# Optimization experiments

Hardware: AMD Instinct MI355X
Metric: run time of the kernel (lower is better)

Reference implementation:

```python
import jax, jax.numpy as jnp
import numpy as np

T, B, I, H, O = 512, 128, 256, 1024, 256


def setup_inputs() -> dict:
    key = jax.random.key(0)
    ks = jax.random.split(key, 16)
    std = 0.02
    inp = {
        "input_seq": jax.random.normal(ks[0], (T, B, I), dtype=jnp.float32),
        # encoder LSTM (torch gate order i, f, g, o)
        "W_ih_enc": jax.random.normal(ks[1], (4 * H, I), dtype=jnp.float32) * std,
        "W_hh_enc": jax.random.normal(ks[2], (4 * H, H), dtype=jnp.float32) * std,
        "b_ih_enc": jnp.zeros((4 * H,), dtype=jnp.float32),
        "b_hh_enc": jnp.zeros((4 * H,), dtype=jnp.float32),
        # attention: Linear(2H -> H) and score vector v
        "W_attn": jax.random.normal(ks[3], (H, 2 * H), dtype=jnp.float32) * std,
        "b_attn": jnp.zeros((H,), dtype=jnp.float32),
        "v": jax.random.uniform(ks[4], (H,), dtype=jnp.float32),
        # decoder LSTMCell (H -> H)
        "W_ih_dec": jax.random.normal(ks[5], (4 * H, H), dtype=jnp.float32) * std,
        "W_hh_dec": jax.random.normal(ks[6], (4 * H, H), dtype=jnp.float32) * std,
        "b_ih_dec": jnp.zeros((4 * H,), dtype=jnp.float32),
        "b_hh_dec": jnp.zeros((4 * H,), dtype=jnp.float32),
        # decoder linear H -> H
        "W_dec": jax.random.normal(ks[7], (H, H), dtype=jnp.float32) * std,
        "b_dec": jnp.zeros((H,), dtype=jnp.float32),
        # top-level output linear H -> O
        "W_out": jax.random.normal(ks[8], (O, H), dtype=jnp.float32) * std,
        "b_out": jnp.zeros((O,), dtype=jnp.float32),
        "len_out": 30,
    }
    return inp


def _lstm_cell(h, c, x, Wih, Whh, bih, bhh):
    gates = x @ Wih.T + bih + h @ Whh.T + bhh  # [B, 4H]
    i, f, g, o = jnp.split(gates, 4, axis=-1)
    i, f, o = jax.nn.sigmoid(i), jax.nn.sigmoid(f), jax.nn.sigmoid(o)
    c = f * c + i * jnp.tanh(g)
    h = o * jnp.tanh(c)
    return h, c


def reference(input_seq, W_ih_enc, W_hh_enc, b_ih_enc, b_hh_enc,
              W_attn, b_attn, v, W_ih_dec, W_hh_dec, b_ih_dec, b_hh_dec,
              W_dec, b_dec, W_out, b_out, len_out):
    Tdim, Bdim, _ = input_seq.shape
    Hdim = W_hh_enc.shape[1]

    # ---- encoder LSTM over time (seq-first) ----
    h0 = jnp.zeros((Bdim, Hdim), dtype=input_seq.dtype)
    c0 = jnp.zeros((Bdim, Hdim), dtype=input_seq.dtype)

    def enc_step(carry, x_t):
        h, c = carry
        h, c = _lstm_cell(h, c, x_t, W_ih_enc, W_hh_enc, b_ih_enc, b_hh_enc)
        return (h, c), h

    (h_enc, _), context_seq = jax.lax.scan(enc_step, (h0, c0), input_seq)
    # dropout is identity in eval mode

    # ---- precompute context part of Bahdanau energy ----
    # W_attn acts on cat([hidden, context]) => split into hidden / context blocks
    W_h, W_c = W_attn[:, :Hdim], W_attn[:, Hdim:]
    ctx_proj = jnp.einsum('tbh,gh->tbg', context_seq, W_c) + b_attn  # [T,B,H]

    def dec_step(carry, _):
        h, c = carry
        energy = jnp.tanh(h @ W_h.T + ctx_proj)          # [T,B,H]
        scores = jnp.einsum('tbh,h->tb', energy, v)       # [T,B]
        w = jax.nn.softmax(scores, axis=0)                # softmax over time
        context = jnp.einsum('tbh,tb->bh', context_seq, w)  # [B,H]
        h, c = _lstm_cell(h, c, context, W_ih_dec, W_hh_dec, b_ih_dec, b_hh_dec)
        out = jax.nn.relu(h @ W_dec.T + b_dec)
        out = out @ W_out.T + b_out
        return (h, c), out

    _, outputs = jax.lax.scan(dec_step, (h_enc, jnp.zeros_like(h_enc)), None,
                              length=len_out)
    return outputs  # [len_out, B, O]
```

## Files before the change

kernel.cpp:

```cpp
#include <hip/hip_runtime.h>
#include <hip/hip_bf16.h>
#include <type_traits>


static constexpr int T_ = 512, B_ = 128, I_ = 256, H_ = 1024, O_ = 256;

typedef unsigned short ushort;
typedef unsigned long long u64;
typedef __attribute__((ext_vector_type(8))) short bf16x8;
typedef __attribute__((ext_vector_type(4))) float f32x4;
typedef __attribute__((ext_vector_type(4))) unsigned uint4_t;
typedef __attribute__((ext_vector_type(8))) _Float16 half8;

__device__ __forceinline__ float bf2f(ushort u) {
    union { unsigned i; float f; } cv; cv.i = ((unsigned)u) << 16; return cv.f;
}
__device__ __forceinline__ ushort f2bf(float f) {
    union { float f; unsigned u; } c; c.f = f;
    unsigned r = c.u + 0x7FFFu + ((c.u >> 16) & 1u);
    return (ushort)(r >> 16);
}
__device__ __forceinline__ float fast_sigmoid(float x) { return 1.f / (1.f + __expf(-x)); }
__device__ __forceinline__ float fast_tanh(float x) {
    float ax = fabsf(x);
    float e = __expf(-2.f * ax);
    float t = (1.f - e) / (1.f + e);
    return copysignf(t, x);
}
__device__ __forceinline__ f32x4 mfma16(bf16x8 a, bf16x8 b, f32x4 c) {
    return __builtin_amdgcn_mfma_f32_16x16x32_bf16(a, b, c, 0, 0, 0);
}
__device__ __forceinline__ bf16x8 ld8(const ushort* p) { return *(const bf16x8*)(const void*)p; }

__device__ __forceinline__ bf16x8 ld8p(const ushort* base, int row, int ko) {
    const size_t t = (size_t)(row >> 7);
    const int b = row & 127;
    const ushort* p0 = base + t * (size_t)(B_ * H_) + ((size_t)((ko >> 2) * B_ + b) << 2);
    union { u64 q[2]; bf16x8 v; } u;
    u.q[0] = *(const u64*)(const void*)p0;
    u.q[1] = *(const u64*)(const void*)(p0 + (B_ << 2));
    return u.v;
}

__device__ __forceinline__ void split8(const float* p, bf16x8& hi, bf16x8& lo) {
    #pragma unroll
    for (int j = 0; j < 8; j++) {
        const float f = p[j];
        const ushort h = f2bf(f);
        hi[j] = (short)h;
        lo[j] = (short)f2bf(f - bf2f(h));
    }
}

__global__ __launch_bounds__(256) void split_w(
    const float* __restrict__ src, int srcld, int coloff,
    ushort* __restrict__ hi, ushort* __restrict__ lo, int K)
{
    const int k = blockIdx.x * 256 + threadIdx.x;
    const int r = blockIdx.y;
    const float f = src[(size_t)r * srcld + coloff + k];
    const ushort h = f2bf(f);
    hi[(size_t)r * K + k] = h;
    lo[(size_t)r * K + k] = f2bf(f - bf2f(h));
}

__global__ __launch_bounds__(256) void pack_x(float* __restrict__ x)
{
    const size_t i = ((size_t)blockIdx.x * 256 + threadIdx.x) * 8;
    float4 a = *(const float4*)(x + i);
    float4 b = *(const float4*)(x + i + 4);
    unsigned w[8];
    const float f_[8] = {a.x, a.y, a.z, a.w, b.x, b.y, b.z, b.w};
    #pragma unroll
    for (int j = 0; j < 8; j++) {
        const ushort h = f2bf(f_[j]);
        const ushort l = f2bf(f_[j] - bf2f(h));
        w[j] = (unsigned)h | ((unsigned)l << 16);
    }
    *(uint4_t*)(void*)(x + i)     = uint4_t{w[0], w[1], w[2], w[3]};
    *(uint4_t*)(void*)(x + i + 4) = uint4_t{w[4], w[5], w[6], w[7]};
}

#define ENC_SMEM_BYTES (32*64*8*2*2 + 8*64*8*2*2 + 16*132*4)
#define LORING_SLOTS 256

__global__ __launch_bounds__(512) void enc_persistent(
    const unsigned* __restrict__ xpk,
    const ushort* __restrict__ WhhE_h, const ushort* __restrict__ WhhE_l,
    const ushort* __restrict__ WihE_h, const ushort* __restrict__ WihE_l,
    const float* __restrict__ bih, const float* __restrict__ bhh,
    const ushort* __restrict__ hzero,
    ushort* __restrict__ ctx_seq,
    ushort* __restrict__ loring,
    ushort* __restrict__ enc_lo_fin,
    unsigned* __restrict__ bar)
{
    extern __shared__ __align__(16) char smem[];
    ushort* LWh = (ushort*)smem;
    ushort* LWl = LWh + 32 * 64 * 8;
    ushort* LIh = LWl + 32 * 64 * 8;
    ushort* LIl = LIh + 8 * 64 * 8;
    float*  Gt  = (float*)(LIl + 8 * 64 * 8);

    const int tid  = threadIdx.x;
    const int wave = tid >> 6, lane = tid & 63;
    const int quad = lane >> 4, l15 = lane & 15;
    const int bx   = blockIdx.x;
    const int h0   = bx << 2;
    const int wr   = ((l15 >> 2) * H_) + h0 + (l15 & 3);

    {
        const size_t woff = (size_t)wr * H_;
        #pragma unroll
        for (int ii = 0; ii < 4; ii++) {
            const int i   = wave + (ii << 3);
            const int src = (i << 5) + (quad << 3);
            *(bf16x8*)(LWh + ((i << 6) + lane) * 8) = ld8(WhhE_h + woff + src);
            *(bf16x8*)(LWl + ((i << 6) + lane) * 8) = ld8(WhhE_l + woff + src);
        }
        const size_t ioff = (size_t)wr * I_;
        const int src2 = (wave << 5) + (quad << 3);
        *(bf16x8*)(LIh + ((wave << 6) + lane) * 8) = ld8(WihE_h + ioff + src2);
        *(bf16x8*)(LIl + ((wave << 6) + lane) * 8) = ld8(WihE_l + ioff + src2);
    }

    const int bl_  = tid >> 2, hl = tid & 3;
    const int hidx = h0 + hl;
    const float bs0 = bih[hidx]           + bhh[hidx];
    const float bs1 = bih[H_ + hidx]      + bhh[H_ + hidx];
    const float bs2 = bih[2 * H_ + hidx]  + bhh[2 * H_ + hidx];
    const float bs3 = bih[3 * H_ + hidx]  + bhh[3 * H_ + hidx];
    float c_reg = 0.f;
    __syncthreads();

    const int arow = (wave << 4) + l15;
    const size_t xoff = (size_t)arow * I_;

    for (int t = 0; t < T_; t++) {
        const unsigned* xs = xpk + (size_t)t * (B_ * I_) + xoff;

        f32x4 acc0 = {0.f, 0.f, 0.f, 0.f}, acc1 = acc0, acc2 = acc0;
        #pragma unroll
        for (int kc = 0; kc < I_; kc += 32) {
            const int i = kc >> 5;
            const bf16x8 bh = *(const bf16x8*)(LIh + ((i << 6) + lane) * 8);
            const bf16x8 bl = *(const bf16x8*)(LIl + ((i << 6) + lane) * 8);
            const uint4_t w0 = *(const uint4_t*)(const void*)(xs + kc + (quad << 3));
            const uint4_t w1 = *(const uint4_t*)(const void*)(xs + kc + (quad << 3) + 4);
            bf16x8 ah, al;
            ah[0] = (short)(w0.x & 0xffff); al[0] = (short)(w0.x >> 16);
            ah[1] = (short)(w0.y & 0xffff); al[1] = (short)(w0.y >> 16);
            ah[2] = (short)(w0.z & 0xffff); al[2] = (short)(w0.z >> 16);
            ah[3] = (short)(w0.w & 0xffff); al[3] = (short)(w0.w >> 16);
            ah[4] = (short)(w1.x & 0xffff); al[4] = (short)(w1.x >> 16);
            ah[5] = (short)(w1.y & 0xffff); al[5] = (short)(w1.y >> 16);
            ah[6] = (short)(w1.z & 0xffff); al[6] = (short)(w1.z >> 16);
            ah[7] = (short)(w1.w & 0xffff); al[7] = (short)(w1.w >> 16);
            acc0 = mfma16(ah, bh, acc0);
            acc1 = mfma16(ah, bl, acc1);
            acc2 = mfma16(al, bh, acc2);
        }

        if (t != 0) {
            if (tid == 0) {
                while (__hip_atomic_load(&bar[0], __ATOMIC_RELAXED,
                                         __HIP_MEMORY_SCOPE_AGENT) < (unsigned)t)
                    __builtin_amdgcn_s_sleep(2);
            }
            __syncthreads();
        }

        const ushort* hi_src = t ? (ctx_seq + (size_t)(t - 1) * (B_ * H_)) : hzero;
        const ushort* lo_src = t ? (loring + (size_t)((t - 1) & (LORING_SLOTS - 1))
                                             * (B_ * H_)) : hzero;
        #pragma unroll 8
        for (int kc = 0; kc < H_; kc += 32) {
            const int i  = kc >> 5;
            const int ko = kc + (quad << 3);
            const bf16x8 bh = *(const bf16x8*)(LWh + ((i << 6) + lane) * 8);
            const bf16x8 bl = *(const bf16x8*)(LWl + ((i << 6) + lane) * 8);
            const bf16x8 ah = ld8p(hi_src, arow, ko);
            const bf16x8 al = ld8p(lo_src, arow, ko);
            acc0 = mfma16(ah, bh, acc0);
            acc1 = mfma16(ah, bl, acc1);
            acc2 = mfma16(al, bh, acc2);
        }
        #pragma unroll
        for (int r = 0; r < 4; r++)
            Gt[l15 * 132 + (wave << 4) + (quad << 2) + r] = acc0[r] + acc1[r] + acc2[r];
        __syncthreads();

        const float gi = Gt[hl * 132 + bl_]        + bs0;
        const float gf = Gt[(4 + hl) * 132 + bl_]  + bs1;
        const float gg = Gt[(8 + hl) * 132 + bl_]  + bs2;
        const float go = Gt[(12 + hl) * 132 + bl_] + bs3;
        const float ig = fast_sigmoid(gi), fg = fast_sigmoid(gf);
        const float gtv = fast_tanh(gg),   og = fast_sigmoid(go);
        c_reg = fg * c_reg + ig * gtv;
        const float hnew = og * fast_tanh(c_reg);
        const ushort hh  = f2bf(hnew);
        const ushort hlo = f2bf(hnew - bf2f(hh));

        const unsigned hp = (unsigned)hh  | (__shfl_down((unsigned)hh, 1)  << 16);
        const unsigned lp = (unsigned)hlo | (__shfl_down((unsigned)hlo, 1) << 16);
        const unsigned pi = ((unsigned)bx << 9) + (unsigned)tid;
        if (!(tid & 1)) {
            __hip_atomic_store((unsigned*)(void*)&ctx_seq[(size_t)t * (B_ * H_) + pi],
                               hp, __ATOMIC_RELAXED, __HIP_MEMORY_SCOPE_AGENT);
            __hip_atomic_store((unsigned*)(void*)
                               &loring[(size_t)(t & (LORING_SLOTS - 1)) * (B_ * H_) + pi],
                               lp, __ATOMIC_RELAXED, __HIP_MEMORY_SCOPE_AGENT);
            if (t == T_ - 1)
                *(unsigned*)(void*)&enc_lo_fin[pi] = lp;
        }

        if (t != T_ - 1) {
            __syncthreads();
            if (tid == 0) {
                const unsigned tgt = (unsigned)(t + 1) * 16u;
                unsigned* leaf = bar + 64 + ((bx & 15) << 4);
                const unsigned la = __hip_atomic_fetch_add(leaf, 1u, __ATOMIC_RELAXED,
                                                           __HIP_MEMORY_SCOPE_AGENT) + 1;
                if (la == tgt) {
                    const unsigned ra = __hip_atomic_fetch_add(&bar[32], 1u,
                                            __ATOMIC_RELAXED, __HIP_MEMORY_SCOPE_AGENT) + 1;
                    if (ra == tgt)
                        __hip_atomic_store(&bar[0], (unsigned)(t + 1),
                                           __ATOMIC_RELAXED, __HIP_MEMORY_SCOPE_AGENT);
                }
            }
        }
    }
}

template<bool WSPLIT, bool XSPLIT, int KX>
__global__ __launch_bounds__(256) void lstm_mfma(
    const ushort* __restrict__ h_hi, const ushort* __restrict__ h_lo,
    const void* __restrict__ x_p, const ushort* __restrict__ x_lo,
    const void* __restrict__ Whh_a, const void* __restrict__ Whh_b,
    const void* __restrict__ Wih_a, const void* __restrict__ Wih_b,
    const float* __restrict__ bih, const float* __restrict__ bhh,
    const float* __restrict__ c_in, float* __restrict__ c_out,
    ushort* __restrict__ h_out_hi, ushort* __restrict__ h_out_lo)
{
    __shared__ float Gt[16][65];
    const int tid = threadIdx.x;
    const int wave = tid >> 6, lane = tid & 63;
    const int quad = lane >> 4, l15 = lane & 15;
    const int h0 = blockIdx.x << 2;
    const int mbase = (blockIdx.y << 6) + (wave << 4);
    const int arow = mbase + l15;
    const int wr = ((l15 >> 2) * H_) + h0 + (l15 & 3);

    f32x4 acc0 = {0.f,0.f,0.f,0.f}, acc1 = acc0, acc2 = acc0;

    {
        const size_t woff = (size_t)wr * H_;
        #pragma unroll 4
        for (int kc = 0; kc < H_; kc += 32) {
            const int ko = kc + quad * 8;
            bf16x8 bh, bl;
            if constexpr (WSPLIT) {
                bh = ld8((const ushort*)Whh_a + woff + ko);
                bl = ld8((const ushort*)Whh_b + woff + ko);
            } else {
                split8((const float*)Whh_a + woff + ko, bh, bl);
            }
            const bf16x8 ah = ld8p(h_hi, arow, ko);
            const bf16x8 al = ld8p(h_lo, arow, ko);
            acc0 = mfma16(ah, bh, acc0);
            acc1 = mfma16(ah, bl, acc1);
            acc2 = mfma16(al, bh, acc2);
        }
    }
    {
        const size_t woff = (size_t)wr * KX;
        #pragma unroll 2
        for (int kc = 0; kc < KX; kc += 32) {
            const int ko = kc + quad * 8;
            bf16x8 bh, bl;
            if constexpr (WSPLIT) {
                bh = ld8((const ushort*)Wih_a + woff + ko);
                bl = ld8((const ushort*)Wih_b + woff + ko);
            } else {
                split8((const float*)Wih_a + woff + ko, bh, bl);
            }
            bf16x8 ah, al;
            if constexpr (XSPLIT) {
                ah = ld8p((const ushort*)x_p, arow, ko);
                al = ld8p(x_lo, arow, ko);
            } else {
                split8((const float*)x_p + (size_t)arow * KX + ko, ah, al);
            }
            acc0 = mfma16(ah, bh, acc0);
            acc1 = mfma16(ah, bl, acc1);
            acc2 = mfma16(al, bh, acc2);
        }
    }
    #pragma unroll
    for (int r = 0; r < 4; r++)
        Gt[l15][(wave << 4) + quad * 4 + r] = acc0[r] + acc1[r] + acc2[r];
    __syncthreads();

    const int bl_ = tid >> 2, hl = tid & 3;
    const int b = (blockIdx.y << 6) + bl_;
    const int hidx = h0 + hl;
    const float gi = Gt[hl][bl_]      + bih[hidx]          + bhh[hidx];
    const float gf = Gt[4 + hl][bl_]  + bih[H_ + hidx]     + bhh[H_ + hidx];
    const float gg = Gt[8 + hl][bl_]  + bih[2 * H_ + hidx] + bhh[2 * H_ + hidx];
    const float go = Gt[12 + hl][bl_] + bih[3 * H_ + hidx] + bhh[3 * H_ + hidx];
    const float ig = fast_sigmoid(gi), fg = fast_sigmoid(gf);
    const float gt = fast_tanh(gg),    og = fast_sigmoid(go);
    const float cold = c_in[b * H_ + hidx];
    const float cnew = fg * cold + ig * gt;
    const float hnew = og * fast_tanh(cnew);
    c_out[b * H_ + hidx] = cnew;
    const ushort hh = f2bf(hnew);
    const size_t op = ((size_t)(hidx >> 2) * B_ + b) * 4 + (hidx & 3);
    h_out_hi[op] = hh;
    h_out_lo[op] = f2bf(hnew - bf2f(hh));
}

template<bool A_LO, int NT, int OM, bool RELU, int K, bool APANEL>
__global__ __launch_bounds__(256) void gemm_mfma(
    const ushort* __restrict__ Ahi, const ushort* __restrict__ Alo, int lda,
    const ushort* __restrict__ Whi, const ushort* __restrict__ Wlo,
    const float* __restrict__ bias,
    void* __restrict__ out0, void* __restrict__ out1, int ldc)
{
    const int tid = threadIdx.x;
    const int wave = tid >> 6, lane = tid & 63;
    const int quad = lane >> 4, l15 = lane & 15;
    const int colbase = (blockIdx.x * NT) << 4;
    const int row = (blockIdx.y << 6) + (wave << 4) + l15;
    const size_t aoff = (size_t)row * lda;

    f32x4 acc0[NT], acc1[NT], acc2[NT];
    #pragma unroll
    for (int nt = 0; nt < NT; nt++) {
        acc0[nt] = {0.f,0.f,0.f,0.f}; acc1[nt] = acc0[nt]; acc2[nt] = acc0[nt];
    }
    size_t woff[NT];
    #pragma unroll
    for (int nt = 0; nt < NT; nt++)
        woff[nt] = (size_t)(colbase + (nt << 4) + l15) * K;

    #pragma unroll 2
    for (int kc = 0; kc < K; kc += 32) {
        const int ko = kc + quad * 8;
        const bf16x8 ah = APANEL ? ld8p(Ahi, row, ko) : ld8(Ahi + aoff + ko);
        bf16x8 al;
        if (A_LO) al = APANEL ? ld8p(Alo, row, ko) : ld8(Alo + aoff + ko);
        #pragma unroll
        for (int nt = 0; nt < NT; nt++) {
            const bf16x8 bh = ld8(Whi + woff[nt] + ko);
            const bf16x8 bl = ld8(Wlo + woff[nt] + ko);
            acc0[nt] = mfma16(ah, bh, acc0[nt]);
            acc1[nt] = mfma16(ah, bl, acc1[nt]);
            if (A_LO) acc2[nt] = mfma16(al, bh, acc2[nt]);
        }
    }
    const size_t orow0 = ((size_t)blockIdx.y << 6) + (wave << 4) + quad * 4;
    const size_t HALF_IDX = (size_t)32768 * 1024;
    #pragma unroll
    for (int nt = 0; nt < NT; nt++) {
        const int col = colbase + (nt << 4) + l15;
        const float bv = bias ? bias[col] : 0.f;
        #pragma unroll
        for (int r = 0; r < 4; r++) {
            float v = acc0[nt][r] + acc1[nt][r] + (A_LO ? acc2[nt][r] : 0.f) + bv;
            if (RELU) v = fmaxf(v, 0.f);
            const size_t idx = (orow0 + r) * (size_t)ldc + col;
            if constexpr (OM == 0) {
                ((float*)out0)[idx] = v;
            } else if constexpr (OM == 3) {
                const size_t idxp = ((size_t)(col >> 2) * B_ + (orow0 + r)) * 4 + (col & 3);
                const ushort h = f2bf(v);
                ((ushort*)out0)[idxp] = h;
                ((ushort*)out1)[idxp] = f2bf(v - bf2f(h));
            } else {
                if (idx < HALF_IDX) ((_Float16*)out0)[idx] = (_Float16)v;
                else                ((_Float16*)out1)[idx - HALF_IDX] = (_Float16)v;
            }
        }
    }
}

__global__ __launch_bounds__(256) void attn_score_kernel(
    const float* __restrict__ q,
    const _Float16* __restrict__ P0, const _Float16* __restrict__ P1,
    const float* __restrict__ v, float* __restrict__ scores)
{
    const int wave = threadIdx.x >> 6, lane = threadIdx.x & 63;
    const int p = (blockIdx.x << 2) + wave;
    const int t = p >> 7, b = p & 127;
    const size_t base = (size_t)(t * B_ + b) * H_ + (lane << 4);
    const size_t HALF_IDX = (size_t)32768 * 1024;
    const _Float16* pp = (base < HALF_IDX) ? (P0 + base) : (P1 + (base - HALF_IDX));

    const half8 u0 = *(const half8*)(const void*)pp;
    const half8 u1 = *(const half8*)(const void*)(pp + 8);
    float pv[16];
    #pragma unroll
    for (int j = 0; j < 8; j++) { pv[j] = (float)u0[j]; pv[8 + j] = (float)u1[j]; }

    const float* qp = q + b * H_ + (lane << 4);
    const float* vp = v + (lane << 4);
    float sum = 0.f;
    #pragma unroll
    for (int j0 = 0; j0 < 16; j0 += 4) {
        const float4 qv = *(const float4*)(qp + j0);
        const float4 vv = *(const float4*)(vp + j0);
        sum += vv.x * fast_tanh(qv.x + pv[j0 + 0]);
        sum += vv.y * fast_tanh(qv.y + pv[j0 + 1]);
        sum += vv.z * fast_tanh(qv.z + pv[j0 + 2]);
        sum += vv.w * fast_tanh(qv.w + pv[j0 + 3]);
    }
    #pragma unroll
    for (int off = 32; off; off >>= 1) sum += __shfl_down(sum, off);
    if (lane == 0) scores[b * T_ + t] = sum;
}

__global__ __launch_bounds__(256) void softmax_kernel(
    const float* __restrict__ scores, float* __restrict__ scT)
{
    __shared__ float red[256];
    const int b = blockIdx.x, tid = threadIdx.x;
    const float s0 = scores[b * T_ + tid];
    const float s1 = scores[b * T_ + tid + 256];
    red[tid] = fmaxf(s0, s1);
    __syncthreads();
    for (int off = 128; off; off >>= 1) {
        if (tid < off) red[tid] = fmaxf(red[tid], red[tid + off]);
        __syncthreads();
    }
    const float mx = red[0];
    __syncthreads();
    const float e0 = __expf(s0 - mx), e1 = __expf(s1 - mx);
    red[tid] = e0 + e1;
    __syncthreads();
    for (int off = 128; off; off >>= 1) {
        if (tid < off) red[tid] += red[tid + off];
        __syncthreads();
    }
    const float inv = 1.f / red[0];
    scT[tid * B_ + b] = e0 * inv;
    scT[(tid + 256) * B_ + b] = e1 * inv;
}

__global__ __launch_bounds__(256) void attn_context_kernel(
    const float* __restrict__ scT, const ushort* __restrict__ ctx,
    ushort* __restrict__ chi, ushort* __restrict__ clo)
{
    const int u = blockIdx.x * 256 + threadIdx.x;
    const int c = u >> 7, b = u & 127;
    const ushort* cp = ctx + ((size_t)(c * B_ + b) << 2);
    const float* wp = scT + b;
    float a0 = 0.f, a1 = 0.f, a2 = 0.f, a3 = 0.f;
    #pragma unroll 4
    for (int t = 0; t < T_; t++) {
        const float w = wp[t << 7];
        const u64 raw = *(const u64*)(const void*)(cp + (size_t)t * (B_ * H_));
        a0 += w * bf2f((ushort)raw);
        a1 += w * bf2f((ushort)(raw >> 16));
        a2 += w * bf2f((ushort)(raw >> 32));
        a3 += w * bf2f((ushort)(raw >> 48));
    }
    const size_t i0 = (size_t)(c * B_ + b) << 2;
    const ushort h0 = f2bf(a0), h1 = f2bf(a1), h2 = f2bf(a2), h3 = f2bf(a3);
    const ushort l0 = f2bf(a0 - bf2f(h0)), l1 = f2bf(a1 - bf2f(h1));
    const ushort l2 = f2bf(a2 - bf2f(h2)), l3 = f2bf(a3 - bf2f(h3));
    *(u64*)(void*)&chi[i0] = (u64)h0 | ((u64)h1 << 16) | ((u64)h2 << 32) | ((u64)h3 << 48);
    *(u64*)(void*)&clo[i0] = (u64)l0 | ((u64)l1 << 16) | ((u64)l2 << 32) | ((u64)l3 << 48);
}

extern "C" void kernel_launch(void* const* d_in, const int* in_sizes, int n_in,
                              void* d_out, int out_size, void* d_ws, size_t ws_size,
                              hipStream_t stream)
{
    const float* input_seq = (const float*)d_in[0];
    const float* W_ih_enc  = (const float*)d_in[1];
    const float* W_hh_enc  = (const float*)d_in[2];
    const float* b_ih_enc  = (const float*)d_in[3];
    const float* b_hh_enc  = (const float*)d_in[4];
    const float* W_attn    = (const float*)d_in[5];
    const float* b_attn    = (const float*)d_in[6];
    const float* v         = (const float*)d_in[7];
    const float* W_ih_dec  = (const float*)d_in[8];
    const float* W_hh_dec  = (const float*)d_in[9];
    const float* b_ih_dec  = (const float*)d_in[10];
    const float* b_hh_dec  = (const float*)d_in[11];
    const float* W_dec     = (const float*)d_in[12];
    const float* b_dec     = (const float*)d_in[13];
    const float* W_out     = (const float*)d_in[14];
    const float* b_out     = (const float*)d_in[15];
    float* out = (float*)d_out;
    const int LEN = out_size / (B_ * O_);
    const int BH = B_ * H_;

    char* ws = (char*)d_ws;
    size_t off = 0;
    auto aus = [&](size_t n) { ushort* p = (ushort*)(ws + off); off += n * 2; return p; };
    auto af  = [&](size_t n) { float*  p = (float*) (ws + off); off += n * 4; return p; };

    ushort* WhhE_h = aus((size_t)4*H_*H_); ushort* WhhE_l = aus((size_t)4*H_*H_);
    ushort* WihE_h = aus((size_t)4*H_*I_); ushort* WihE_l = aus((size_t)4*H_*I_);
    ushort* Wh_h   = aus((size_t)H_*H_);   ushort* Wh_l   = aus((size_t)H_*H_);
    ushort* Wc_h   = aus((size_t)H_*H_);   ushort* Wc_l   = aus((size_t)H_*H_);
    ushort* Wdec_h = aus((size_t)H_*H_);   ushort* Wdec_l = aus((size_t)H_*H_);
    ushort* Wout_h = aus((size_t)O_*H_);   ushort* Wout_l = aus((size_t)O_*H_);

    ushort* ctx_seq = aus((size_t)T_ * BH);
    ushort* hzero   = aus(BH);
    ushort* enc_lo_fin = aus(BH);
    ushort* hd_hi0  = aus(BH); ushort* hd_hi1  = aus(BH);
    ushort* hd_lo0  = aus(BH); ushort* hd_lo1  = aus(BH);
    ushort* ctx_hi  = aus(BH); ushort* ctx_lo  = aus(BH);
    ushort* d1_hi   = aus(BH); ushort* d1_lo   = aus(BH);
    float*  cbuf    = af(BH);
    float*  qbuf    = af(BH);
    float*  scores  = af(B_ * T_);
    float*  scT     = af(B_ * T_);
    unsigned* barbuf = (unsigned*)(ws + off); off += 4096;

    ushort* loring = aus((size_t)LORING_SLOTS * BH);
    const size_t P_HALF = (size_t)(T_ / 2) * BH * 2;
    _Float16* P1 = (_Float16*)loring;
    _Float16* P0;
    if (ws_size >= off + P_HALF) {
        P0 = (_Float16*)(ws + off);
    } else {
        P0 = (_Float16*)const_cast<float*>(input_seq);
    }

    auto spl = [&](const float* src, int srcld, int coloff, ushort* hi, ushort* lo,
                   int R, int K) {
        split_w<<<dim3(K / 256, R), 256, 0, stream>>>(src, srcld, coloff, hi, lo, K);
    };
    spl(W_hh_enc, H_,     0,  WhhE_h, WhhE_l, 4 * H_, H_);
    spl(W_ih_enc, I_,     0,  WihE_h, WihE_l, 4 * H_, I_);
    spl(W_attn,   2 * H_, 0,  Wh_h,   Wh_l,   H_,     H_);
    spl(W_attn,   2 * H_, H_, Wc_h,   Wc_l,   H_,     H_);
    spl(W_dec,    H_,     0,  Wdec_h, Wdec_l, H_,     H_);
    spl(W_out,    H_,     0,  Wout_h, Wout_l, O_,     H_);

    pack_x<<<(T_ * B_ * I_) / (256 * 8), 256, 0, stream>>>(
        const_cast<float*>(input_seq));

    hipMemsetAsync(hzero,  0, (size_t)BH * 2, stream);
    hipMemsetAsync(barbuf, 0, 4096, stream);

    enc_persistent<<<dim3(H_ / 4), 512, ENC_SMEM_BYTES, stream>>>(
        (const unsigned*)input_seq, WhhE_h, WhhE_l, WihE_h, WihE_l,
        b_ih_enc, b_hh_enc, hzero, ctx_seq, loring, enc_lo_fin, barbuf);

    gemm_mfma<false, 8, 4, false, H_, true><<<dim3(8, (T_ * B_) / 64), 256, 0, stream>>>(
        ctx_seq, nullptr, H_, Wc_h, Wc_l, b_attn, P0, P1, H_);

    hipMemsetAsync(cbuf, 0, (size_t)BH * 4, stream);
    ushort* dhh[2] = {hd_hi0, hd_hi1};
    ushort* dhl[2] = {hd_lo0, hd_lo1};
    for (int s = 0; s < LEN; s++) {
        const ushort* hi_in = (s == 0) ? ctx_seq + (size_t)(T_ - 1) * BH : dhh[s & 1];
        const ushort* lo_in = (s == 0) ? enc_lo_fin : dhl[s & 1];

        gemm_mfma<true, 1, 0, false, H_, true><<<dim3(H_ / 16, 2), 256, 0, stream>>>(
            hi_in, lo_in, H_, Wh_h, Wh_l, nullptr, qbuf, nullptr, H_);
        attn_score_kernel<<<T_ * B_ / 4, 256, 0, stream>>>(qbuf, P0, P1, v, scores);
        softmax_kernel<<<B_, 256, 0, stream>>>(scores, scT);
        attn_context_kernel<<<BH / 4 / 256, 256, 0, stream>>>(scT, ctx_seq, ctx_hi, ctx_lo);
        lstm_mfma<false, true, H_><<<dim3(H_ / 4, 2), 256, 0, stream>>>(
            hi_in, lo_in, (const void*)ctx_hi, ctx_lo,
            W_hh_dec, nullptr, W_ih_dec, nullptr, b_ih_dec, b_hh_dec,
            cbuf, cbuf, dhh[(s + 1) & 1], dhl[(s + 1) & 1]);
        gemm_mfma<true, 1, 3, true, H_, true><<<dim3(H_ / 16, 2), 256, 0, stream>>>(
            dhh[(s + 1) & 1], dhl[(s + 1) & 1], H_, Wdec_h, Wdec_l, b_dec,
            d1_hi, d1_lo, H_);
        gemm_mfma<true, 1, 0, false, H_, true><<<dim3(O_ / 16, 2), 256, 0, stream>>>(
            d1_hi, d1_lo, H_, Wout_h, Wout_l, b_out,
            out + (size_t)s * B_ * O_, nullptr, O_);
    }
    (void)in_sizes; (void)n_in;
}
```

Measured before the change: 16.71 ms.

## Split encoder K-reduction across two wave groups and split attention context over time

The persistent encoder kernel now runs 1024 threads per block. Two groups of 8 waves each reduce half of the input and hidden K dimensions, and their partial gate sums are added through a doubled shared-memory tile before the LSTM update. Separately, the decoder's attention-context reduction over time is split into two halves that run as twice as many blocks, with a small finishing kernel that sums them and converts to hi/lo bf16. This is meant to shorten the serial per-step latency on the encoder's critical path and to raise parallelism in the context reduction. It costs more threads and shared memory per block, possible register pressure under the 1024 launch bound, and an extra kernel launch per decoder step.

New measurement: 14.30 ms. -14.4%, faster.

```diff
diff --git a/kernel.cpp b/kernel.cpp
--- a/kernel.cpp
+++ b/kernel.cpp
@@ -81,10 +81,10 @@
     *(uint4_t*)(void*)(x + i + 4) = uint4_t{w[4], w[5], w[6], w[7]};
 }
 
-#define ENC_SMEM_BYTES (32*64*8*2*2 + 8*64*8*2*2 + 16*132*4)
+#define ENC_SMEM_BYTES (32*64*8*2*2 + 8*64*8*2*2 + 2*16*132*4)
 #define LORING_SLOTS 256
 
-__global__ __launch_bounds__(512) void enc_persistent(
+__global__ __launch_bounds__(1024) void enc_persistent(
     const unsigned* __restrict__ xpk,
     const ushort* __restrict__ WhhE_h, const ushort* __restrict__ WhhE_l,
     const ushort* __restrict__ WihE_h, const ushort* __restrict__ WihE_l,
@@ -105,6 +105,8 @@
     const int tid  = threadIdx.x;
     const int wave = tid >> 6, lane = tid & 63;
     const int quad = lane >> 4, l15 = lane & 15;
+    const int rt   = wave & 7;
+    const int kw   = wave >> 3;
     const int bx   = blockIdx.x;
     const int h0   = bx << 2;
     const int wr   = ((l15 >> 2) * H_) + h0 + (l15 & 3);
@@ -112,16 +114,18 @@
     {
         const size_t woff = (size_t)wr * H_;
         #pragma unroll
-        for (int ii = 0; ii < 4; ii++) {
-            const int i   = wave + (ii << 3);
+        for (int ii = 0; ii < 2; ii++) {
+            const int i   = (ii << 4) + wave;
             const int src = (i << 5) + (quad << 3);
             *(bf16x8*)(LWh + ((i << 6) + lane) * 8) = ld8(WhhE_h + woff + src);
             *(bf16x8*)(LWl + ((i << 6) + lane) * 8) = ld8(WhhE_l + woff + src);
         }
-        const size_t ioff = (size_t)wr * I_;
-        const int src2 = (wave << 5) + (quad << 3);
-        *(bf16x8*)(LIh + ((wave << 6) + lane) * 8) = ld8(WihE_h + ioff + src2);
-        *(bf16x8*)(LIl + ((wave << 6) + lane) * 8) = ld8(WihE_l + ioff + src2);
+        if (wave < 8) {
+            const size_t ioff = (size_t)wr * I_;
+            const int src2 = (wave << 5) + (quad << 3);
+            *(bf16x8*)(LIh + ((wave << 6) + lane) * 8) = ld8(WihE_h + ioff + src2);
+            *(bf16x8*)(LIl + ((wave << 6) + lane) * 8) = ld8(WihE_l + ioff + src2);
+        }
     }
 
     const int bl_  = tid >> 2, hl = tid & 3;
@@ -133,15 +137,18 @@
     float c_reg = 0.f;
     __syncthreads();
 
-    const int arow = (wave << 4) + l15;
+    const int arow = (rt << 4) + l15;
     const size_t xoff = (size_t)arow * I_;
+    const int kx0 = kw << 7;
+    const int kh0 = kw << 9;
 
     for (int t = 0; t < T_; t++) {
         const unsigned* xs = xpk + (size_t)t * (B_ * I_) + xoff;
 
         f32x4 acc0 = {0.f, 0.f, 0.f, 0.f}, acc1 = acc0, acc2 = acc0;
         #pragma unroll
-        for (int kc = 0; kc < I_; kc += 32) {
+        for (int kk = 0; kk < 128; kk += 32) {
+            const int kc = kx0 + kk;
             const int i = kc >> 5;
             const bf16x8 bh = *(const bf16x8*)(LIh + ((i << 6) + lane) * 8);
             const bf16x8 bl = *(const bf16x8*)(LIl + ((i << 6) + lane) * 8);
@@ -174,7 +181,8 @@
         const ushort* lo_src = t ? (loring + (size_t)((t - 1) & (LORING_SLOTS - 1))
                                              * (B_ * H_)) : hzero;
         #pragma unroll 8
-        for (int kc = 0; kc < H_; kc += 32) {
+        for (int kk = 0; kk < 512; kk += 32) {
+            const int kc = kh0 + kk;
             const int i  = kc >> 5;
             const int ko = kc + (quad << 3);
             const bf16x8 bh = *(const bf16x8*)(LWh + ((i << 6) + lane) * 8);
@@ -187,24 +195,27 @@
         }
         #pragma unroll
         for (int r = 0; r < 4; r++)
-            Gt[l15 * 132 + (wave << 4) + (quad << 2) + r] = acc0[r] + acc1[r] + acc2[r];
+            Gt[kw * (16 * 132) + l15 * 132 + (rt << 4) + (quad << 2) + r] =
+                acc0[r] + acc1[r] + acc2[r];
         __syncthreads();
 
-        const float gi = Gt[hl * 132 + bl_]        + bs0;
-        const float gf = Gt[(4 + hl) * 132 + bl_]  + bs1;
-        const float gg = Gt[(8 + hl) * 132 + bl_]  + bs2;
-        const float go = Gt[(12 + hl) * 132 + bl_] + bs3;
-        const float ig = fast_sigmoid(gi), fg = fast_sigmoid(gf);
-        const float gtv = fast_tanh(gg),   og = fast_sigmoid(go);
-        c_reg = fg * c_reg + ig * gtv;
-        const float hnew = og * fast_tanh(c_reg);
-        const ushort hh  = f2bf(hnew);
-        const ushort hlo = f2bf(hnew - bf2f(hh));
-
+        ushort hh = 0, hlo = 0;
+        if (tid < 512) {
+            const float gi = Gt[hl * 132 + bl_]        + Gt[16*132 + hl * 132 + bl_]        + bs0;
+            const float gf = Gt[(4 + hl) * 132 + bl_]  + Gt[16*132 + (4 + hl) * 132 + bl_]  + bs1;
+            const float gg = Gt[(8 + hl) * 132 + bl_]  + Gt[16*132 + (8 + hl) * 132 + bl_]  + bs2;
+            const float go = Gt[(12 + hl) * 132 + bl_] + Gt[16*132 + (12 + hl) * 132 + bl_] + bs3;
+            const float ig = fast_sigmoid(gi), fg = fast_sigmoid(gf);
+            const float gtv = fast_tanh(gg),   og = fast_sigmoid(go);
+            c_reg = fg * c_reg + ig * gtv;
+            const float hnew = og * fast_tanh(c_reg);
+            hh  = f2bf(hnew);
+            hlo = f2bf(hnew - bf2f(hh));
+        }
         const unsigned hp = (unsigned)hh  | (__shfl_down((unsigned)hh, 1)  << 16);
         const unsigned lp = (unsigned)hlo | (__shfl_down((unsigned)hlo, 1) << 16);
-        const unsigned pi = ((unsigned)bx << 9) + (unsigned)tid;
-        if (!(tid & 1)) {
+        if (tid < 512 && !(tid & 1)) {
+            const unsigned pi = ((unsigned)bx << 9) + (unsigned)tid;
             __hip_atomic_store((unsigned*)(void*)&ctx_seq[(size_t)t * (B_ * H_) + pi],
                                hp, __ATOMIC_RELAXED, __HIP_MEMORY_SCOPE_AGENT);
             __hip_atomic_store((unsigned*)(void*)
@@ -448,17 +459,20 @@
     scT[(tid + 256) * B_ + b] = e1 * inv;
 }
 
-__global__ __launch_bounds__(256) void attn_context_kernel(
+__global__ __launch_bounds__(256) void attn_context_part(
     const float* __restrict__ scT, const ushort* __restrict__ ctx,
-    ushort* __restrict__ chi, ushort* __restrict__ clo)
+    float* __restrict__ pctx)
 {
     const int u = blockIdx.x * 256 + threadIdx.x;
-    const int c = u >> 7, b = u & 127;
-    const ushort* cp = ctx + ((size_t)(c * B_ + b) << 2);
-    const float* wp = scT + b;
+    const int cb = u & 32767;
+    const int half = u >> 15;
+    const int c = cb >> 7, b = cb & 127;
+    const ushort* cp = ctx + ((size_t)(c * B_ + b) << 2)
+                           + (size_t)(half << 8) * (B_ * H_);
+    const float* wp = scT + ((half << 8) * B_) + b;
     float a0 = 0.f, a1 = 0.f, a2 = 0.f, a3 = 0.f;
     #pragma unroll 4
-    for (int t = 0; t < T_; t++) {
+    for (int t = 0; t < 256; t++) {
         const float w = wp[t << 7];
         const u64 raw = *(const u64*)(const void*)(cp + (size_t)t * (B_ * H_));
         a0 += w * bf2f((ushort)raw);
@@ -466,7 +480,20 @@
         a2 += w * bf2f((ushort)(raw >> 32));
         a3 += w * bf2f((ushort)(raw >> 48));
     }
-    const size_t i0 = (size_t)(c * B_ + b) << 2;
+    float4 o = {a0, a1, a2, a3};
+    *(float4*)(void*)(pctx + ((size_t)(cb << 1) + half) * 4) = o;
+}
+
+__global__ __launch_bounds__(256) void attn_context_fin(
+    const float* __restrict__ pctx,
+    ushort* __restrict__ chi, ushort* __restrict__ clo)
+{
+    const int cb = blockIdx.x * 256 + threadIdx.x;
+    const float4 x0 = *(const float4*)(pctx + (size_t)cb * 8);
+    const float4 x1 = *(const float4*)(pctx + (size_t)cb * 8 + 4);
+    const float a0 = x0.x + x1.x, a1 = x0.y + x1.y;
+    const float a2 = x0.z + x1.z, a3 = x0.w + x1.w;
+    const size_t i0 = (size_t)cb << 2;
     const ushort h0 = f2bf(a0), h1 = f2bf(a1), h2 = f2bf(a2), h3 = f2bf(a3);
     const ushort l0 = f2bf(a0 - bf2f(h0)), l1 = f2bf(a1 - bf2f(h1));
     const ushort l2 = f2bf(a2 - bf2f(h2)), l3 = f2bf(a3 - bf2f(h3));
@@ -521,6 +548,7 @@
     float*  qbuf    = af(BH);
     float*  scores  = af(B_ * T_);
     float*  scT     = af(B_ * T_);
+    float*  pctx    = af((size_t)32768 * 8);
     unsigned* barbuf = (unsigned*)(ws + off); off += 4096;
 
     ushort* loring = aus((size_t)LORING_SLOTS * BH);
@@ -550,7 +578,7 @@
     hipMemsetAsync(hzero,  0, (size_t)BH * 2, stream);
     hipMemsetAsync(barbuf, 0, 4096, stream);
 
-    enc_persistent<<<dim3(H_ / 4), 512, ENC_SMEM_BYTES, stream>>>(
+    enc_persistent<<<dim3(H_ / 4), 1024, ENC_SMEM_BYTES, stream>>>(
         (const unsigned*)input_seq, WhhE_h, WhhE_l, WihE_h, WihE_l,
         b_ih_enc, b_hh_enc, hzero, ctx_seq, loring, enc_lo_fin, barbuf);
 
@@ -568,7 +596,8 @@
             hi_in, lo_in, H_, Wh_h, Wh_l, nullptr, qbuf, nullptr, H_);
         attn_score_kernel<<<T_ * B_ / 4, 256, 0, stream>>>(qbuf, P0, P1, v, scores);
         softmax_kernel<<<B_, 256, 0, stream>>>(scores, scT);
-        attn_context_kernel<<<BH / 4 / 256, 256, 0, stream>>>(scT, ctx_seq, ctx_hi, ctx_lo);
+        attn_context_part<<<256, 256, 0, stream>>>(scT, ctx_seq, pctx);
+        attn_context_fin<<<128, 256, 0, stream>>>(pctx, ctx_hi, ctx_lo);
         lstm_mfma<false, true, H_><<<dim3(H_ / 4, 2), 256, 0, stream>>>(
             hi_in, lo_in, (const void*)ctx_hi, ctx_lo,
             W_hh_dec, nullptr, W_ih_dec, nullptr, b_ih_dec, b_hh_dec,
```
